# Performance work log

Measured on AMD Instinct MI355X. Metric: run time of the kernel, lower is better.

Reference implementation:

```python
import jax, jax.numpy as jnp
import numpy as np

B, N, D, H = 2, 2048, 1024, 16
DH = D // H
SCALE = DH ** -0.5

def setup_inputs() -> dict:
    key = jax.random.key(0)
    k1, k2, k3 = jax.random.split(key, 3)
    x = jax.random.normal(k1, (B, N, D), dtype=jnp.float32)
    W_qkv = jax.random.normal(k2, (3 * D, D), dtype=jnp.float32) * (D ** -0.5)
    W_out = jax.random.normal(k3, (D, D), dtype=jnp.float32) * (D ** -0.5)
    mask = jnp.tril(jnp.ones((N, N), dtype=jnp.int32))  # causal mask; 0 -> -inf
    return {"x": x, "mask": mask, "W_qkv": W_qkv, "W_out": W_out}

def reference(x, mask, W_qkv, W_out):
    b, n, d = x.shape
    qkv = x @ W_qkv.T                                   # [B,N,3D]
    qkv = qkv.reshape(b, n, 3, H, DH).transpose(2, 0, 3, 1, 4)  # [3,B,H,N,DH]
    q, k, v = qkv[0], qkv[1], qkv[2]
    attn = jnp.einsum('bhqd,bhkd->bhqk', q, k) * SCALE  # [B,H,N,N]
    attn = jnp.where(mask == 0, -jnp.inf, attn)
    attn = jax.nn.softmax(attn, axis=-1)
    out = jnp.einsum('bhqk,bhkd->bhqd', attn, v)        # [B,H,N,DH]
    out = out.transpose(0, 2, 1, 3).reshape(b, n, d)    # [B,N,D]
    return out @ W_out.T
```

## Files before the change

kernel.cpp:

```cpp
#include <hip/hip_runtime.h>
#include <hip/hip_bf16.h>


typedef __hip_bfloat16 bf16;
typedef short bf16x8 __attribute__((ext_vector_type(8)));
typedef short bf16x4 __attribute__((ext_vector_type(4)));
typedef float f32x4 __attribute__((ext_vector_type(4)));

#define QSCALE 0.1803368801111204f

typedef __attribute__((address_space(3))) unsigned int lds_u32;
typedef const __attribute__((address_space(1))) unsigned int glob_u32;

__device__ __forceinline__ void glds16(const void* g, void* l) {
    __builtin_amdgcn_global_load_lds((glob_u32*)g, (lds_u32*)l, 16, 0, 0);
}

__device__ __forceinline__ short f2bf(float f) {
    __hip_bfloat16 h = __float2bfloat16(f);
    return *reinterpret_cast<short*>(&h);
}

__device__ __forceinline__ unsigned pack_bf16(float a, float b) {
    unsigned au = __builtin_bit_cast(unsigned, a) + 0x8000u;
    unsigned bu = __builtin_bit_cast(unsigned, b) + 0x8000u;
    return __builtin_amdgcn_perm(bu, au, 0x07060302u);
}

__global__ void cast_all(const float* __restrict__ x, const float* __restrict__ wqkv,
                         const float* __restrict__ wout,
                         bf16* __restrict__ xb, bf16* __restrict__ wqkvb,
                         bf16* __restrict__ woutb) {
    int i = blockIdx.x * blockDim.x + threadIdx.x;
    const float4* s; short4* d; int o;
    if (i < 1048576)               { s = (const float4*)x;    d = (short4*)xb;    o = i; }
    else if (i < 1835008)          { s = (const float4*)wqkv; d = (short4*)wqkvb; o = i - 1048576; }
    else                           { s = (const float4*)wout; d = (short4*)woutb; o = i - 1835008; }
    float4 f = s[o];
    short4 v;
    v.x = f2bf(f.x); v.y = f2bf(f.y); v.z = f2bf(f.z); v.w = f2bf(f.w);
    d[o] = v;
}

template<int EPI>
__global__ __launch_bounds__(256)
void gemm128(const bf16* __restrict__ A, const bf16* __restrict__ Bt,
             float* __restrict__ Cf,
             bf16* __restrict__ qp, bf16* __restrict__ kp, bf16* __restrict__ vp,
             int K, int Ncols) {
    __shared__ alignas(16) short As[2][4096];
    __shared__ alignas(16) short Bs[2][4096];

    const int tid = threadIdx.x;
    const int wave = tid >> 6, lane = tid & 63;
    const int quad = lane >> 4, l16 = lane & 15;
    const int wm = wave >> 1, wn = wave & 1;
    const int m0 = blockIdx.x * 128;
    const int n0 = blockIdx.y * 128;

    f32x4 acc[4][4] = {};

    const int srow = tid >> 2;
    const int skk  = (((tid & 3) ^ ((tid >> 3) & 3))) * 8;
    const bf16* Ag = A  + (size_t)(m0 + srow) * K + skk;
    const bf16* Bg = Bt + (size_t)(n0 + srow) * K + skk;
    const size_t rowskip = (size_t)64 * K;
    short* Asl = &As[0][0] + tid * 8;
    short* Bsl = &Bs[0][0] + tid * 8;

    const int xk = (quad ^ ((l16 >> 1) & 3)) * 8;
    const int arow = wm * 64 + l16;
    const int brow = wn * 64 + l16;

    const int KI = K >> 5;
    glds16(Ag, Asl);
    glds16(Ag + rowskip, Asl + 2048);
    glds16(Bg, Bsl);
    glds16(Bg + rowskip, Bsl + 2048);
    __syncthreads();

    int buf = 0;
    for (int ki = 0; ki < KI; ++ki) {
        if (ki + 1 < KI) {
            const bf16* ag = Ag + (ki + 1) * 32;
            const bf16* bg = Bg + (ki + 1) * 32;
            short* ad = Asl + (buf ^ 1) * 4096;
            short* bd = Bsl + (buf ^ 1) * 4096;
            glds16(ag, ad);
            glds16(ag + rowskip, ad + 2048);
            glds16(bg, bd);
            glds16(bg + rowskip, bd + 2048);
        }
        const short* ab = &As[buf][0];
        const short* bb = &Bs[buf][0];
        bf16x8 af[4], bf[4];
        #pragma unroll
        for (int mt = 0; mt < 4; ++mt)
            af[mt] = *reinterpret_cast<const bf16x8*>(ab + (arow + mt * 16) * 32 + xk);
        #pragma unroll
        for (int nt = 0; nt < 4; ++nt)
            bf[nt] = *reinterpret_cast<const bf16x8*>(bb + (brow + nt * 16) * 32 + xk);
        #pragma unroll
        for (int mt = 0; mt < 4; ++mt)
            #pragma unroll
            for (int nt = 0; nt < 4; ++nt)
                acc[mt][nt] = __builtin_amdgcn_mfma_f32_16x16x32_bf16(
                    af[mt], bf[nt], acc[mt][nt], 0, 0, 0);
        __syncthreads();
        buf ^= 1;
    }

    #pragma unroll
    for (int mt = 0; mt < 4; ++mt) {
        #pragma unroll
        for (int nt = 0; nt < 4; ++nt) {
            #pragma unroll
            for (int r = 0; r < 4; ++r) {
                int gm = m0 + wm * 64 + mt * 16 + quad * 4 + r;
                int gn = n0 + wn * 64 + nt * 16 + l16;
                float val = acc[mt][nt][r];
                if (EPI == 0) {
                    int sel = gn >> 10, rem = gn & 1023;
                    int h = rem >> 6, dh = rem & 63;
                    int b = gm >> 11, nq = gm & 2047;
                    if (sel == 0) val *= QSCALE;
                    bf16* dst = (sel == 0) ? qp : ((sel == 1) ? kp : vp);
                    dst[((((size_t)b * 16 + h) * 2048) + nq) * 64 + dh] = __float2bfloat16(val);
                } else {
                    Cf[(size_t)gm * Ncols + gn] = val;
                }
            }
        }
    }
}

__global__ __launch_bounds__(256)
void flash_attn(const bf16* __restrict__ Q, const bf16* __restrict__ K,
                const bf16* __restrict__ V, bf16* __restrict__ O) {
    __shared__ alignas(16) short Ks[2][64][72];
    __shared__ alignas(16) short Vt[2][64][68];

    const int tid = threadIdx.x;
    const int wave = tid >> 6, lane = tid & 63;
    const int quad = lane >> 4, l16 = lane & 15;
    const int bh = blockIdx.x;
    const int yy = blockIdx.y;
    const int qt = (yy < 8) ? yy : (15 - (yy & 7));
    const int Q0 = qt * 128;
    const float NEG_INF = -__builtin_inff();

    const bf16* Qb = Q + (size_t)bh * 2048 * 64;
    const bf16* Kb = K + (size_t)bh * 2048 * 64;
    const bf16* Vb = V + (size_t)bh * 2048 * 64;

    const int qrowA = Q0 + wave * 16 + l16;
    const int qrowB = qrowA + 64;
    const bf16x8 qfA0 = *reinterpret_cast<const bf16x8*>(Qb + (size_t)qrowA * 64 + quad * 8);
    const bf16x8 qfA1 = *reinterpret_cast<const bf16x8*>(Qb + (size_t)qrowA * 64 + 32 + quad * 8);
    const bf16x8 qfB0 = *reinterpret_cast<const bf16x8*>(Qb + (size_t)qrowB * 64 + quad * 8);
    const bf16x8 qfB1 = *reinterpret_cast<const bf16x8*>(Qb + (size_t)qrowB * 64 + 32 + quad * 8);

    float lA = 0.f, lB = 0.f;
    f32x4 oA[4] = {}, oB[4] = {};

    const int krow = tid >> 2;
    const int kcol = (tid & 3) * 16;
    const int kb = (tid & 15) * 4;
    const int db = (tid >> 4) * 4;

    {
        bf16x8 a0 = *reinterpret_cast<const bf16x8*>(Kb + (size_t)krow * 64 + kcol);
        bf16x8 a1 = *reinterpret_cast<const bf16x8*>(Kb + (size_t)krow * 64 + kcol + 8);
        bf16x4 L0 = *reinterpret_cast<const bf16x4*>(Vb + (size_t)(kb + 0) * 64 + db);
        bf16x4 L1 = *reinterpret_cast<const bf16x4*>(Vb + (size_t)(kb + 1) * 64 + db);
        bf16x4 L2 = *reinterpret_cast<const bf16x4*>(Vb + (size_t)(kb + 2) * 64 + db);
        bf16x4 L3 = *reinterpret_cast<const bf16x4*>(Vb + (size_t)(kb + 3) * 64 + db);
        *reinterpret_cast<bf16x8*>(&Ks[0][krow][kcol]) = a0;
        *reinterpret_cast<bf16x8*>(&Ks[0][krow][kcol + 8]) = a1;
        #pragma unroll
        for (int j = 0; j < 4; ++j) {
            bf16x4 w; w[0] = L0[j]; w[1] = L1[j]; w[2] = L2[j]; w[3] = L3[j];
            *reinterpret_cast<bf16x4*>(&Vt[0][db + j][kb]) = w;
        }
    }
    __syncthreads();

    int buf = 0;
    for (int j0 = 0; j0 < Q0; j0 += 64) {
        const bf16* Kn = Kb + (size_t)(j0 + 64) * 64;
        const bf16* Vn = Vb + (size_t)(j0 + 64) * 64;
        bf16x8 nk0 = *reinterpret_cast<const bf16x8*>(Kn + (size_t)krow * 64 + kcol);
        bf16x8 nk1 = *reinterpret_cast<const bf16x8*>(Kn + (size_t)krow * 64 + kcol + 8);
        bf16x4 N0 = *reinterpret_cast<const bf16x4*>(Vn + (size_t)(kb + 0) * 64 + db);
        bf16x4 N1 = *reinterpret_cast<const bf16x4*>(Vn + (size_t)(kb + 1) * 64 + db);
        bf16x4 N2 = *reinterpret_cast<const bf16x4*>(Vn + (size_t)(kb + 2) * 64 + db);
        bf16x4 N3 = *reinterpret_cast<const bf16x4*>(Vn + (size_t)(kb + 3) * 64 + db);

        bf16x4 pkA[4], pkB[4];
        #pragma unroll
        for (int t = 0; t < 4; ++t) {
            bf16x8 k0 = *reinterpret_cast<const bf16x8*>(&Ks[buf][16 * t + l16][quad * 8]);
            bf16x8 k1 = *reinterpret_cast<const bf16x8*>(&Ks[buf][16 * t + l16][32 + quad * 8]);
            f32x4 sA = {}, sB = {};
            sA = __builtin_amdgcn_mfma_f32_16x16x32_bf16(k0, qfA0, sA, 0, 0, 0);
            sA = __builtin_amdgcn_mfma_f32_16x16x32_bf16(k1, qfA1, sA, 0, 0, 0);
            sB = __builtin_amdgcn_mfma_f32_16x16x32_bf16(k0, qfB0, sB, 0, 0, 0);
            sB = __builtin_amdgcn_mfma_f32_16x16x32_bf16(k1, qfB1, sB, 0, 0, 0);
            float a0 = __builtin_amdgcn_exp2f(sA[0]);
            float a1 = __builtin_amdgcn_exp2f(sA[1]);
            float a2 = __builtin_amdgcn_exp2f(sA[2]);
            float a3 = __builtin_amdgcn_exp2f(sA[3]);
            float b0 = __builtin_amdgcn_exp2f(sB[0]);
            float b1 = __builtin_amdgcn_exp2f(sB[1]);
            float b2 = __builtin_amdgcn_exp2f(sB[2]);
            float b3 = __builtin_amdgcn_exp2f(sB[3]);
            lA += (a0 + a1) + (a2 + a3);
            lB += (b0 + b1) + (b2 + b3);
            unsigned* pa = reinterpret_cast<unsigned*>(&pkA[t]);
            pa[0] = pack_bf16(a0, a1); pa[1] = pack_bf16(a2, a3);
            unsigned* pb = reinterpret_cast<unsigned*>(&pkB[t]);
            pb[0] = pack_bf16(b0, b1); pb[1] = pack_bf16(b2, b3);
        }

        #pragma unroll
        for (int t = 0; t < 4; ++t) {
            #pragma unroll
            for (int dt = 0; dt < 4; ++dt) {
                bf16x4 vf = *reinterpret_cast<const bf16x4*>(
                    &Vt[buf][dt * 16 + l16][t * 16 + quad * 4]);
                oA[dt] = __builtin_amdgcn_mfma_f32_16x16x16bf16_1k(vf, pkA[t], oA[dt], 0, 0, 0);
                oB[dt] = __builtin_amdgcn_mfma_f32_16x16x16bf16_1k(vf, pkB[t], oB[dt], 0, 0, 0);
            }
        }

        *reinterpret_cast<bf16x8*>(&Ks[buf ^ 1][krow][kcol]) = nk0;
        *reinterpret_cast<bf16x8*>(&Ks[buf ^ 1][krow][kcol + 8]) = nk1;
        #pragma unroll
        for (int j = 0; j < 4; ++j) {
            bf16x4 w; w[0] = N0[j]; w[1] = N1[j]; w[2] = N2[j]; w[3] = N3[j];
            *reinterpret_cast<bf16x4*>(&Vt[buf ^ 1][db + j][kb]) = w;
        }
        __syncthreads();
        buf ^= 1;
    }

    {
        const bf16* Kn = Kb + (size_t)(Q0 + 64) * 64;
        const bf16* Vn = Vb + (size_t)(Q0 + 64) * 64;
        bf16x8 nk0 = *reinterpret_cast<const bf16x8*>(Kn + (size_t)krow * 64 + kcol);
        bf16x8 nk1 = *reinterpret_cast<const bf16x8*>(Kn + (size_t)krow * 64 + kcol + 8);
        bf16x4 N0 = *reinterpret_cast<const bf16x4*>(Vn + (size_t)(kb + 0) * 64 + db);
        bf16x4 N1 = *reinterpret_cast<const bf16x4*>(Vn + (size_t)(kb + 1) * 64 + db);
        bf16x4 N2 = *reinterpret_cast<const bf16x4*>(Vn + (size_t)(kb + 2) * 64 + db);
        bf16x4 N3 = *reinterpret_cast<const bf16x4*>(Vn + (size_t)(kb + 3) * 64 + db);

        bf16x4 pkA[4], pkB[4];
        #pragma unroll
        for (int t = 0; t < 4; ++t) {
            bf16x8 k0 = *reinterpret_cast<const bf16x8*>(&Ks[buf][16 * t + l16][quad * 8]);
            bf16x8 k1 = *reinterpret_cast<const bf16x8*>(&Ks[buf][16 * t + l16][32 + quad * 8]);
            f32x4 sB = {};
            sB = __builtin_amdgcn_mfma_f32_16x16x32_bf16(k0, qfB0, sB, 0, 0, 0);
            sB = __builtin_amdgcn_mfma_f32_16x16x32_bf16(k1, qfB1, sB, 0, 0, 0);
            float b0 = __builtin_amdgcn_exp2f(sB[0]);
            float b1 = __builtin_amdgcn_exp2f(sB[1]);
            float b2 = __builtin_amdgcn_exp2f(sB[2]);
            float b3 = __builtin_amdgcn_exp2f(sB[3]);
            lB += (b0 + b1) + (b2 + b3);
            unsigned* pb = reinterpret_cast<unsigned*>(&pkB[t]);
            pb[0] = pack_bf16(b0, b1); pb[1] = pack_bf16(b2, b3);
            if (t <= wave) {
                f32x4 sA = {};
                sA = __builtin_amdgcn_mfma_f32_16x16x32_bf16(k0, qfA0, sA, 0, 0, 0);
                sA = __builtin_amdgcn_mfma_f32_16x16x32_bf16(k1, qfA1, sA, 0, 0, 0);
                if (t == wave) {
                    #pragma unroll
                    for (int r = 0; r < 4; ++r)
                        if (quad * 4 + r > l16) sA[r] = NEG_INF;
                }
                float a0 = __builtin_amdgcn_exp2f(sA[0]);
                float a1 = __builtin_amdgcn_exp2f(sA[1]);
                float a2 = __builtin_amdgcn_exp2f(sA[2]);
                float a3 = __builtin_amdgcn_exp2f(sA[3]);
                lA += (a0 + a1) + (a2 + a3);
                unsigned* pa = reinterpret_cast<unsigned*>(&pkA[t]);
                pa[0] = pack_bf16(a0, a1); pa[1] = pack_bf16(a2, a3);
            }
        }
        #pragma unroll
        for (int t = 0; t < 4; ++t) {
            #pragma unroll
            for (int dt = 0; dt < 4; ++dt) {
                bf16x4 vf = *reinterpret_cast<const bf16x4*>(
                    &Vt[buf][dt * 16 + l16][t * 16 + quad * 4]);
                oB[dt] = __builtin_amdgcn_mfma_f32_16x16x16bf16_1k(vf, pkB[t], oB[dt], 0, 0, 0);
                if (t <= wave)
                    oA[dt] = __builtin_amdgcn_mfma_f32_16x16x16bf16_1k(vf, pkA[t], oA[dt], 0, 0, 0);
            }
        }

        *reinterpret_cast<bf16x8*>(&Ks[buf ^ 1][krow][kcol]) = nk0;
        *reinterpret_cast<bf16x8*>(&Ks[buf ^ 1][krow][kcol + 8]) = nk1;
        #pragma unroll
        for (int j = 0; j < 4; ++j) {
            bf16x4 w; w[0] = N0[j]; w[1] = N1[j]; w[2] = N2[j]; w[3] = N3[j];
            *reinterpret_cast<bf16x4*>(&Vt[buf ^ 1][db + j][kb]) = w;
        }
        __syncthreads();
        buf ^= 1;
    }

    {
        bf16x4 pkB[4];
        #pragma unroll
        for (int t = 0; t < 4; ++t) {
            if (t <= wave) {
                bf16x8 k0 = *reinterpret_cast<const bf16x8*>(&Ks[buf][16 * t + l16][quad * 8]);
                bf16x8 k1 = *reinterpret_cast<const bf16x8*>(&Ks[buf][16 * t + l16][32 + quad * 8]);
                f32x4 sB = {};
                sB = __builtin_amdgcn_mfma_f32_16x16x32_bf16(k0, qfB0, sB, 0, 0, 0);
                sB = __builtin_amdgcn_mfma_f32_16x16x32_bf16(k1, qfB1, sB, 0, 0, 0);
                if (t == wave) {
                    #pragma unroll
                    for (int r = 0; r < 4; ++r)
                        if (quad * 4 + r > l16) sB[r] = NEG_INF;
                }
                float b0 = __builtin_amdgcn_exp2f(sB[0]);
                float b1 = __builtin_amdgcn_exp2f(sB[1]);
                float b2 = __builtin_amdgcn_exp2f(sB[2]);
                float b3 = __builtin_amdgcn_exp2f(sB[3]);
                lB += (b0 + b1) + (b2 + b3);
                unsigned* pb = reinterpret_cast<unsigned*>(&pkB[t]);
                pb[0] = pack_bf16(b0, b1); pb[1] = pack_bf16(b2, b3);
            }
        }
        #pragma unroll
        for (int t = 0; t < 4; ++t) {
            if (t <= wave) {
                #pragma unroll
                for (int dt = 0; dt < 4; ++dt) {
                    bf16x4 vf = *reinterpret_cast<const bf16x4*>(
                        &Vt[buf][dt * 16 + l16][t * 16 + quad * 4]);
                    oB[dt] = __builtin_amdgcn_mfma_f32_16x16x16bf16_1k(vf, pkB[t], oB[dt], 0, 0, 0);
                }
            }
        }
    }

    lA += __shfl_xor(lA, 16, 64);
    lA += __shfl_xor(lA, 32, 64);
    lB += __shfl_xor(lB, 16, 64);
    lB += __shfl_xor(lB, 32, 64);
    const float invA = 1.f / lA;
    const float invB = 1.f / lB;

    const int b = bh >> 4, h = bh & 15;
    bf16* orowA = O + ((size_t)b * 2048 + qrowA) * 1024 + h * 64;
    bf16* orowB = O + ((size_t)b * 2048 + qrowB) * 1024 + h * 64;
    #pragma unroll
    for (int dt = 0; dt < 4; ++dt) {
        bf16x4 wA, wB;
        unsigned* ua = reinterpret_cast<unsigned*>(&wA);
        ua[0] = pack_bf16(oA[dt][0] * invA, oA[dt][1] * invA);
        ua[1] = pack_bf16(oA[dt][2] * invA, oA[dt][3] * invA);
        *reinterpret_cast<bf16x4*>(orowA + dt * 16 + quad * 4) = wA;
        unsigned* ub = reinterpret_cast<unsigned*>(&wB);
        ub[0] = pack_bf16(oB[dt][0] * invB, oB[dt][1] * invB);
        ub[1] = pack_bf16(oB[dt][2] * invB, oB[dt][3] * invB);
        *reinterpret_cast<bf16x4*>(orowB + dt * 16 + quad * 4) = wB;
    }
}

extern "C" void kernel_launch(void* const* d_in, const int* in_sizes, int n_in,
                              void* d_out, int out_size, void* d_ws, size_t ws_size,
                              hipStream_t stream) {
    const float* x    = (const float*)d_in[0];
    const float* Wqkv = (const float*)d_in[2];
    const float* Wout = (const float*)d_in[3];
    float* out = (float*)d_out;

    char* ws = (char*)d_ws;
    bf16* x_bf    = (bf16*)(ws);
    bf16* wqkv_bf = (bf16*)(ws + 8388608);
    bf16* wout_bf = (bf16*)(ws + 14680064);
    bf16* q       = (bf16*)(ws + 16777216);
    bf16* k       = (bf16*)(ws + 25165824);
    bf16* v       = (bf16*)(ws + 33554432);
    bf16* ao      = (bf16*)(ws + 41943040);

    cast_all<<<8192, 256, 0, stream>>>(x, Wqkv, Wout, x_bf, wqkv_bf, wout_bf);
    gemm128<0><<<dim3(32, 24), 256, 0, stream>>>(x_bf, wqkv_bf, nullptr, q, k, v, 1024, 3072);
    flash_attn<<<dim3(32, 16), 256, 0, stream>>>(q, k, v, ao);
    gemm128<1><<<dim3(32, 8), 256, 0, stream>>>(ao, wout_bf, out, nullptr, nullptr, nullptr, 1024, 1024);
}
```

Before: 181.3 us.

## Split flash attention query tile across 8 waves, separate K/V loader threads

The attention block grows from 256 to 512 threads, so each wave now owns 16 query rows instead of 32 (two row groups A and B). Half the threads load and transpose V while the other half load K, instead of every thread doing both. This halves per-wave register state and serial MFMA work, which should raise latency hiding through more waves per block. The cost is more waves contending for barriers and less reuse of each K/V LDS fragment per wave.

```diff
diff --git a/kernel.cpp b/kernel.cpp
--- a/kernel.cpp
+++ b/kernel.cpp
@@ -134,7 +134,7 @@
     }
 }
 
-__global__ __launch_bounds__(256)
+__global__ __launch_bounds__(512)
 void flash_attn(const bf16* __restrict__ Q, const bf16* __restrict__ K,
                 const bf16* __restrict__ V, bf16* __restrict__ O) {
     __shared__ alignas(16) short Ks[2][64][72];
@@ -153,34 +153,35 @@
     const bf16* Kb = K + (size_t)bh * 2048 * 64;
     const bf16* Vb = V + (size_t)bh * 2048 * 64;
 
-    const int qrowA = Q0 + wave * 16 + l16;
-    const int qrowB = qrowA + 64;
-    const bf16x8 qfA0 = *reinterpret_cast<const bf16x8*>(Qb + (size_t)qrowA * 64 + quad * 8);
-    const bf16x8 qfA1 = *reinterpret_cast<const bf16x8*>(Qb + (size_t)qrowA * 64 + 32 + quad * 8);
-    const bf16x8 qfB0 = *reinterpret_cast<const bf16x8*>(Qb + (size_t)qrowB * 64 + quad * 8);
-    const bf16x8 qfB1 = *reinterpret_cast<const bf16x8*>(Qb + (size_t)qrowB * 64 + 32 + quad * 8);
-
-    float lA = 0.f, lB = 0.f;
-    f32x4 oA[4] = {}, oB[4] = {};
-
-    const int krow = tid >> 2;
-    const int kcol = (tid & 3) * 16;
-    const int kb = (tid & 15) * 4;
-    const int db = (tid >> 4) * 4;
+    const int qrow = Q0 + wave * 16 + l16;
+    const bf16x8 qf0 = *reinterpret_cast<const bf16x8*>(Qb + (size_t)qrow * 64 + quad * 8);
+    const bf16x8 qf1 = *reinterpret_cast<const bf16x8*>(Qb + (size_t)qrow * 64 + 32 + quad * 8);
+
+    float l = 0.f;
+    f32x4 o[4] = {};
+
+    const int t2   = tid & 255;
+    const int krow = t2 >> 2;
+    const int kcol = (t2 & 3) * 16;
+    const int kb   = (t2 & 15) * 4;
+    const int db   = (t2 >> 4) * 4;
 
     {
-        bf16x8 a0 = *reinterpret_cast<const bf16x8*>(Kb + (size_t)krow * 64 + kcol);
-        bf16x8 a1 = *reinterpret_cast<const bf16x8*>(Kb + (size_t)krow * 64 + kcol + 8);
-        bf16x4 L0 = *reinterpret_cast<const bf16x4*>(Vb + (size_t)(kb + 0) * 64 + db);
-        bf16x4 L1 = *reinterpret_cast<const bf16x4*>(Vb + (size_t)(kb + 1) * 64 + db);
-        bf16x4 L2 = *reinterpret_cast<const bf16x4*>(Vb + (size_t)(kb + 2) * 64 + db);
-        bf16x4 L3 = *reinterpret_cast<const bf16x4*>(Vb + (size_t)(kb + 3) * 64 + db);
-        *reinterpret_cast<bf16x8*>(&Ks[0][krow][kcol]) = a0;
-        *reinterpret_cast<bf16x8*>(&Ks[0][krow][kcol + 8]) = a1;
-        #pragma unroll
-        for (int j = 0; j < 4; ++j) {
-            bf16x4 w; w[0] = L0[j]; w[1] = L1[j]; w[2] = L2[j]; w[3] = L3[j];
-            *reinterpret_cast<bf16x4*>(&Vt[0][db + j][kb]) = w;
+        if (tid < 256) {
+            bf16x4 L0 = *reinterpret_cast<const bf16x4*>(Vb + (size_t)(kb + 0) * 64 + db);
+            bf16x4 L1 = *reinterpret_cast<const bf16x4*>(Vb + (size_t)(kb + 1) * 64 + db);
+            bf16x4 L2 = *reinterpret_cast<const bf16x4*>(Vb + (size_t)(kb + 2) * 64 + db);
+            bf16x4 L3 = *reinterpret_cast<const bf16x4*>(Vb + (size_t)(kb + 3) * 64 + db);
+            #pragma unroll
+            for (int j = 0; j < 4; ++j) {
+                bf16x4 w; w[0] = L0[j]; w[1] = L1[j]; w[2] = L2[j]; w[3] = L3[j];
+                *reinterpret_cast<bf16x4*>(&Vt[0][db + j][kb]) = w;
+            }
+        } else {
+            bf16x8 a0 = *reinterpret_cast<const bf16x8*>(Kb + (size_t)krow * 64 + kcol);
+            bf16x8 a1 = *reinterpret_cast<const bf16x8*>(Kb + (size_t)krow * 64 + kcol + 8);
+            *reinterpret_cast<bf16x8*>(&Ks[0][krow][kcol]) = a0;
+            *reinterpret_cast<bf16x8*>(&Ks[0][krow][kcol + 8]) = a1;
         }
     }
     __syncthreads();
@@ -189,37 +190,33 @@
     for (int j0 = 0; j0 < Q0; j0 += 64) {
         const bf16* Kn = Kb + (size_t)(j0 + 64) * 64;
         const bf16* Vn = Vb + (size_t)(j0 + 64) * 64;
-        bf16x8 nk0 = *reinterpret_cast<const bf16x8*>(Kn + (size_t)krow * 64 + kcol);
-        bf16x8 nk1 = *reinterpret_cast<const bf16x8*>(Kn + (size_t)krow * 64 + kcol + 8);
-        bf16x4 N0 = *reinterpret_cast<const bf16x4*>(Vn + (size_t)(kb + 0) * 64 + db);
-        bf16x4 N1 = *reinterpret_cast<const bf16x4*>(Vn + (size_t)(kb + 1) * 64 + db);
-        bf16x4 N2 = *reinterpret_cast<const bf16x4*>(Vn + (size_t)(kb + 2) * 64 + db);
-        bf16x4 N3 = *reinterpret_cast<const bf16x4*>(Vn + (size_t)(kb + 3) * 64 + db);
-
-        bf16x4 pkA[4], pkB[4];
+        bf16x8 nk0, nk1;
+        bf16x4 N0, N1, N2, N3;
+        if (tid < 256) {
+            N0 = *reinterpret_cast<const bf16x4*>(Vn + (size_t)(kb + 0) * 64 + db);
+            N1 = *reinterpret_cast<const bf16x4*>(Vn + (size_t)(kb + 1) * 64 + db);
+            N2 = *reinterpret_cast<const bf16x4*>(Vn + (size_t)(kb + 2) * 64 + db);
+            N3 = *reinterpret_cast<const bf16x4*>(Vn + (size_t)(kb + 3) * 64 + db);
+        } else {
+            nk0 = *reinterpret_cast<const bf16x8*>(Kn + (size_t)krow * 64 + kcol);
+            nk1 = *reinterpret_cast<const bf16x8*>(Kn + (size_t)krow * 64 + kcol + 8);
+        }
+
+        bf16x4 pk[4];
         #pragma unroll
         for (int t = 0; t < 4; ++t) {
             bf16x8 k0 = *reinterpret_cast<const bf16x8*>(&Ks[buf][16 * t + l16][quad * 8]);
             bf16x8 k1 = *reinterpret_cast<const bf16x8*>(&Ks[buf][16 * t + l16][32 + quad * 8]);
-            f32x4 sA = {}, sB = {};
-            sA = __builtin_amdgcn_mfma_f32_16x16x32_bf16(k0, qfA0, sA, 0, 0, 0);
-            sA = __builtin_amdgcn_mfma_f32_16x16x32_bf16(k1, qfA1, sA, 0, 0, 0);
-            sB = __builtin_amdgcn_mfma_f32_16x16x32_bf16(k0, qfB0, sB, 0, 0, 0);
-            sB = __builtin_amdgcn_mfma_f32_16x16x32_bf16(k1, qfB1, sB, 0, 0, 0);
-            float a0 = __builtin_amdgcn_exp2f(sA[0]);
-            float a1 = __builtin_amdgcn_exp2f(sA[1]);
-            float a2 = __builtin_amdgcn_exp2f(sA[2]);
-            float a3 = __builtin_amdgcn_exp2f(sA[3]);
-            float b0 = __builtin_amdgcn_exp2f(sB[0]);
-            float b1 = __builtin_amdgcn_exp2f(sB[1]);
-            float b2 = __builtin_amdgcn_exp2f(sB[2]);
-            float b3 = __builtin_amdgcn_exp2f(sB[3]);
-            lA += (a0 + a1) + (a2 + a3);
-            lB += (b0 + b1) + (b2 + b3);
-            unsigned* pa = reinterpret_cast<unsigned*>(&pkA[t]);
-            pa[0] = pack_bf16(a0, a1); pa[1] = pack_bf16(a2, a3);
-            unsigned* pb = reinterpret_cast<unsigned*>(&pkB[t]);
-            pb[0] = pack_bf16(b0, b1); pb[1] = pack_bf16(b2, b3);
+            f32x4 s = {};
+            s = __builtin_amdgcn_mfma_f32_16x16x32_bf16(k0, qf0, s, 0, 0, 0);
+            s = __builtin_amdgcn_mfma_f32_16x16x32_bf16(k1, qf1, s, 0, 0, 0);
+            float e0 = __builtin_amdgcn_exp2f(s[0]);
+            float e1 = __builtin_amdgcn_exp2f(s[1]);
+            float e2 = __builtin_amdgcn_exp2f(s[2]);
+            float e3 = __builtin_amdgcn_exp2f(s[3]);
+            l += (e0 + e1) + (e2 + e3);
+            unsigned* p = reinterpret_cast<unsigned*>(&pk[t]);
+            p[0] = pack_bf16(e0, e1); p[1] = pack_bf16(e2, e3);
         }
 
         #pragma unroll
@@ -228,17 +225,19 @@
             for (int dt = 0; dt < 4; ++dt) {
                 bf16x4 vf = *reinterpret_cast<const bf16x4*>(
                     &Vt[buf][dt * 16 + l16][t * 16 + quad * 4]);
-                oA[dt] = __builtin_amdgcn_mfma_f32_16x16x16bf16_1k(vf, pkA[t], oA[dt], 0, 0, 0);
-                oB[dt] = __builtin_amdgcn_mfma_f32_16x16x16bf16_1k(vf, pkB[t], oB[dt], 0, 0, 0);
-            }
-        }
-
-        *reinterpret_cast<bf16x8*>(&Ks[buf ^ 1][krow][kcol]) = nk0;
-        *reinterpret_cast<bf16x8*>(&Ks[buf ^ 1][krow][kcol + 8]) = nk1;
-        #pragma unroll
-        for (int j = 0; j < 4; ++j) {
-            bf16x4 w; w[0] = N0[j]; w[1] = N1[j]; w[2] = N2[j]; w[3] = N3[j];
-            *reinterpret_cast<bf16x4*>(&Vt[buf ^ 1][db + j][kb]) = w;
+                o[dt] = __builtin_amdgcn_mfma_f32_16x16x16bf16_1k(vf, pk[t], o[dt], 0, 0, 0);
+            }
+        }
+
+        if (tid < 256) {
+            #pragma unroll
+            for (int j = 0; j < 4; ++j) {
+                bf16x4 w; w[0] = N0[j]; w[1] = N1[j]; w[2] = N2[j]; w[3] = N3[j];
+                *reinterpret_cast<bf16x4*>(&Vt[buf ^ 1][db + j][kb]) = w;
+            }
+        } else {
+            *reinterpret_cast<bf16x8*>(&Ks[buf ^ 1][krow][kcol]) = nk0;
+            *reinterpret_cast<bf16x8*>(&Ks[buf ^ 1][krow][kcol + 8]) = nk1;
         }
         __syncthreads();
         buf ^= 1;
@@ -247,127 +246,119 @@
     {
         const bf16* Kn = Kb + (size_t)(Q0 + 64) * 64;
         const bf16* Vn = Vb + (size_t)(Q0 + 64) * 64;
-        bf16x8 nk0 = *reinterpret_cast<const bf16x8*>(Kn + (size_t)krow * 64 + kcol);
-        bf16x8 nk1 = *reinterpret_cast<const bf16x8*>(Kn + (size_t)krow * 64 + kcol + 8);
-        bf16x4 N0 = *reinterpret_cast<const bf16x4*>(Vn + (size_t)(kb + 0) * 64 + db);
-        bf16x4 N1 = *reinterpret_cast<const bf16x4*>(Vn + (size_t)(kb + 1) * 64 + db);
-        bf16x4 N2 = *reinterpret_cast<const bf16x4*>(Vn + (size_t)(kb + 2) * 64 + db);
-        bf16x4 N3 = *reinterpret_cast<const bf16x4*>(Vn + (size_t)(kb + 3) * 64 + db);
-
-        bf16x4 pkA[4], pkB[4];
-        #pragma unroll
-        for (int t = 0; t < 4; ++t) {
-            bf16x8 k0 = *reinterpret_cast<const bf16x8*>(&Ks[buf][16 * t + l16][quad * 8]);
-            bf16x8 k1 = *reinterpret_cast<const bf16x8*>(&Ks[buf][16 * t + l16][32 + quad * 8]);
-            f32x4 sB = {};
-            sB = __builtin_amdgcn_mfma_f32_16x16x32_bf16(k0, qfB0, sB, 0, 0, 0);
-            sB = __builtin_amdgcn_mfma_f32_16x16x32_bf16(k1, qfB1, sB, 0, 0, 0);
-            float b0 = __builtin_amdgcn_exp2f(sB[0]);
-            float b1 = __builtin_amdgcn_exp2f(sB[1]);
-            float b2 = __builtin_amdgcn_exp2f(sB[2]);
-            float b3 = __builtin_amdgcn_exp2f(sB[3]);
-            lB += (b0 + b1) + (b2 + b3);
-            unsigned* pb = reinterpret_cast<unsigned*>(&pkB[t]);
-            pb[0] = pack_bf16(b0, b1); pb[1] = pack_bf16(b2, b3);
-            if (t <= wave) {
-                f32x4 sA = {};
-                sA = __builtin_amdgcn_mfma_f32_16x16x32_bf16(k0, qfA0, sA, 0, 0, 0);
-                sA = __builtin_amdgcn_mfma_f32_16x16x32_bf16(k1, qfA1, sA, 0, 0, 0);
-                if (t == wave) {
+        bf16x8 nk0, nk1;
+        bf16x4 N0, N1, N2, N3;
+        if (tid < 256) {
+            N0 = *reinterpret_cast<const bf16x4*>(Vn + (size_t)(kb + 0) * 64 + db);
+            N1 = *reinterpret_cast<const bf16x4*>(Vn + (size_t)(kb + 1) * 64 + db);
+            N2 = *reinterpret_cast<const bf16x4*>(Vn + (size_t)(kb + 2) * 64 + db);
+            N3 = *reinterpret_cast<const bf16x4*>(Vn + (size_t)(kb + 3) * 64 + db);
+        } else {
+            nk0 = *reinterpret_cast<const bf16x8*>(Kn + (size_t)krow * 64 + kcol);
+            nk1 = *reinterpret_cast<const bf16x8*>(Kn + (size_t)krow * 64 + kcol + 8);
+        }
+
+        const bool full = (wave >= 4);
+        bf16x4 pk[4];
+        #pragma unroll
+        for (int t = 0; t < 4; ++t) {
+            if (full || t <= wave) {
+                bf16x8 k0 = *reinterpret_cast<const bf16x8*>(&Ks[buf][16 * t + l16][quad * 8]);
+                bf16x8 k1 = *reinterpret_cast<const bf16x8*>(&Ks[buf][16 * t + l16][32 + quad * 8]);
+                f32x4 s = {};
+                s = __builtin_amdgcn_mfma_f32_16x16x32_bf16(k0, qf0, s, 0, 0, 0);
+                s = __builtin_amdgcn_mfma_f32_16x16x32_bf16(k1, qf1, s, 0, 0, 0);
+                if (!full && t == wave) {
                     #pragma unroll
                     for (int r = 0; r < 4; ++r)
-                        if (quad * 4 + r > l16) sA[r] = NEG_INF;
-                }
-                float a0 = __builtin_amdgcn_exp2f(sA[0]);
-                float a1 = __builtin_amdgcn_exp2f(sA[1]);
-                float a2 = __builtin_amdgcn_exp2f(sA[2]);
-                float a3 = __builtin_amdgcn_exp2f(sA[3]);
-                lA += (a0 + a1) + (a2 + a3);
-                unsigned* pa = reinterpret_cast<unsigned*>(&pkA[t]);
-                pa[0] = pack_bf16(a0, a1); pa[1] = pack_bf16(a2, a3);
-            }
-        }
-        #pragma unroll
-        for (int t = 0; t < 4; ++t) {
-            #pragma unroll
-            for (int dt = 0; dt < 4; ++dt) {
-                bf16x4 vf = *reinterpret_cast<const bf16x4*>(
-                    &Vt[buf][dt * 16 + l16][t * 16 + quad * 4]);
-                oB[dt] = __builtin_amdgcn_mfma_f32_16x16x16bf16_1k(vf, pkB[t], oB[dt], 0, 0, 0);
-                if (t <= wave)
-                    oA[dt] = __builtin_amdgcn_mfma_f32_16x16x16bf16_1k(vf, pkA[t], oA[dt], 0, 0, 0);
-            }
-        }
-
-        *reinterpret_cast<bf16x8*>(&Ks[buf ^ 1][krow][kcol]) = nk0;
-        *reinterpret_cast<bf16x8*>(&Ks[buf ^ 1][krow][kcol + 8]) = nk1;
-        #pragma unroll
-        for (int j = 0; j < 4; ++j) {
-            bf16x4 w; w[0] = N0[j]; w[1] = N1[j]; w[2] = N2[j]; w[3] = N3[j];
-            *reinterpret_cast<bf16x4*>(&Vt[buf ^ 1][db + j][kb]) = w;
-        }
-        __syncthreads();
-        buf ^= 1;
-    }
-
-    {
-        bf16x4 pkB[4];
-        #pragma unroll
-        for (int t = 0; t < 4; ++t) {
-            if (t <= wave) {
-                bf16x8 k0 = *reinterpret_cast<const bf16x8*>(&Ks[buf][16 * t + l16][quad * 8]);
-                bf16x8 k1 = *reinterpret_cast<const bf16x8*>(&Ks[buf][16 * t + l16][32 + quad * 8]);
-                f32x4 sB = {};
-                sB = __builtin_amdgcn_mfma_f32_16x16x32_bf16(k0, qfB0, sB, 0, 0, 0);
-                sB = __builtin_amdgcn_mfma_f32_16x16x32_bf16(k1, qfB1, sB, 0, 0, 0);
-                if (t == wave) {
-                    #pragma unroll
-                    for (int r = 0; r < 4; ++r)
-                        if (quad * 4 + r > l16) sB[r] = NEG_INF;
-                }
-                float b0 = __builtin_amdgcn_exp2f(sB[0]);
-                float b1 = __builtin_amdgcn_exp2f(sB[1]);
-                float b2 = __builtin_amdgcn_exp2f(sB[2]);
-                float b3 = __builtin_amdgcn_exp2f(sB[3]);
-                lB += (b0 + b1) + (b2 + b3);
-                unsigned* pb = reinterpret_cast<unsigned*>(&pkB[t]);
-                pb[0] = pack_bf16(b0, b1); pb[1] = pack_bf16(b2, b3);
-            }
-        }
-        #pragma unroll
-        for (int t = 0; t < 4; ++t) {
-            if (t <= wave) {
+                        if (quad * 4 + r > l16) s[r] = NEG_INF;
+                }
+                float e0 = __builtin_amdgcn_exp2f(s[0]);
+                float e1 = __builtin_amdgcn_exp2f(s[1]);
+                float e2 = __builtin_amdgcn_exp2f(s[2]);
+                float e3 = __builtin_amdgcn_exp2f(s[3]);
+                l += (e0 + e1) + (e2 + e3);
+                unsigned* p = reinterpret_cast<unsigned*>(&pk[t]);
+                p[0] = pack_bf16(e0, e1); p[1] = pack_bf16(e2, e3);
+            }
+        }
+        #pragma unroll
+        for (int t = 0; t < 4; ++t) {
+            if (full || t <= wave) {
                 #pragma unroll
                 for (int dt = 0; dt < 4; ++dt) {
                     bf16x4 vf = *reinterpret_cast<const bf16x4*>(
                         &Vt[buf][dt * 16 + l16][t * 16 + quad * 4]);
-                    oB[dt] = __builtin_amdgcn_mfma_f32_16x16x16bf16_1k(vf, pkB[t], oB[dt], 0, 0, 0);
-                }
-            }
-        }
-    }
-
-    lA += __shfl_xor(lA, 16, 64);
-    lA += __shfl_xor(lA, 32, 64);
-    lB += __shfl_xor(lB, 16, 64);
-    lB += __shfl_xor(lB, 32, 64);
-    const float invA = 1.f / lA;
-    const float invB = 1.f / lB;
+                    o[dt] = __builtin_amdgcn_mfma_f32_16x16x16bf16_1k(vf, pk[t], o[dt], 0, 0, 0);
+                }
+            }
+        }
+
+        if (tid < 256) {
+            #pragma unroll
+            for (int j = 0; j < 4; ++j) {
+                bf16x4 w; w[0] = N0[j]; w[1] = N1[j]; w[2] = N2[j]; w[3] = N3[j];
+                *reinterpret_cast<bf16x4*>(&Vt[buf ^ 1][db + j][kb]) = w;
+            }
+        } else {
+            *reinterpret_cast<bf16x8*>(&Ks[buf ^ 1][krow][kcol]) = nk0;
+            *reinterpret_cast<bf16x8*>(&Ks[buf ^ 1][krow][kcol + 8]) = nk1;
+        }
+        __syncthreads();
+        buf ^= 1;
+    }
+
+    if (wave >= 4) {
+        const int w4 = wave - 4;
+        bf16x4 pk[4];
+        #pragma unroll
+        for (int t = 0; t < 4; ++t) {
+            if (t <= w4) {
+                bf16x8 k0 = *reinterpret_cast<const bf16x8*>(&Ks[buf][16 * t + l16][quad * 8]);
+                bf16x8 k1 = *reinterpret_cast<const bf16x8*>(&Ks[buf][16 * t + l16][32 + quad * 8]);
+                f32x4 s = {};
+                s = __builtin_amdgcn_mfma_f32_16x16x32_bf16(k0, qf0, s, 0, 0, 0);
+                s = __builtin_amdgcn_mfma_f32_16x16x32_bf16(k1, qf1, s, 0, 0, 0);
+                if (t == w4) {
+                    #pragma unroll
+                    for (int r = 0; r < 4; ++r)
+                        if (quad * 4 + r > l16) s[r] = NEG_INF;
+                }
+                float e0 = __builtin_amdgcn_exp2f(s[0]);
+                float e1 = __builtin_amdgcn_exp2f(s[1]);
+                float e2 = __builtin_amdgcn_exp2f(s[2]);
+                float e3 = __builtin_amdgcn_exp2f(s[3]);
+                l += (e0 + e1) + (e2 + e3);
+                unsigned* p = reinterpret_cast<unsigned*>(&pk[t]);
+                p[0] = pack_bf16(e0, e1); p[1] = pack_bf16(e2, e3);
+            }
+        }
+        #pragma unroll
+        for (int t = 0; t < 4; ++t) {
+            if (t <= w4) {
+                #pragma unroll
+                for (int dt = 0; dt < 4; ++dt) {
+                    bf16x4 vf = *reinterpret_cast<const bf16x4*>(
+                        &Vt[buf][dt * 16 + l16][t * 16 + quad * 4]);
+                    o[dt] = __builtin_amdgcn_mfma_f32_16x16x16bf16_1k(vf, pk[t], o[dt], 0, 0, 0);
+                }
+            }
+        }
+    }
+
+    l += __shfl_xor(l, 16, 64);
+    l += __shfl_xor(l, 32, 64);
+    const float inv = 1.f / l;
 
     const int b = bh >> 4, h = bh & 15;
-    bf16* orowA = O + ((size_t)b * 2048 + qrowA) * 1024 + h * 64;
-    bf16* orowB = O + ((size_t)b * 2048 + qrowB) * 1024 + h * 64;
+    bf16* orow = O + ((size_t)b * 2048 + qrow) * 1024 + h * 64;
     #pragma unroll
     for (int dt = 0; dt < 4; ++dt) {
-        bf16x4 wA, wB;
-        unsigned* ua = reinterpret_cast<unsigned*>(&wA);
-        ua[0] = pack_bf16(oA[dt][0] * invA, oA[dt][1] * invA);
-        ua[1] = pack_bf16(oA[dt][2] * invA, oA[dt][3] * invA);
-        *reinterpret_cast<bf16x4*>(orowA + dt * 16 + quad * 4) = wA;
-        unsigned* ub = reinterpret_cast<unsigned*>(&wB);
-        ub[0] = pack_bf16(oB[dt][0] * invB, oB[dt][1] * invB);
-        ub[1] = pack_bf16(oB[dt][2] * invB, oB[dt][3] * invB);
-        *reinterpret_cast<bf16x4*>(orowB + dt * 16 + quad * 4) = wB;
+        bf16x4 w;
+        unsigned* u = reinterpret_cast<unsigned*>(&w);
+        u[0] = pack_bf16(o[dt][0] * inv, o[dt][1] * inv);
+        u[1] = pack_bf16(o[dt][2] * inv, o[dt][3] * inv);
+        *reinterpret_cast<bf16x4*>(orow + dt * 16 + quad * 4) = w;
     }
 }
 
@@ -390,6 +381,6 @@
 
     cast_all<<<8192, 256, 0, stream>>>(x, Wqkv, Wout, x_bf, wqkv_bf, wout_bf);
     gemm128<0><<<dim3(32, 24), 256, 0, stream>>>(x_bf, wqkv_bf, nullptr, q, k, v, 1024, 3072);
-    flash_attn<<<dim3(32, 16), 256, 0, stream>>>(q, k, v, ao);
+    flash_attn<<<dim3(32, 16), 512, 0, stream>>>(q, k, v, ao);
     gemm128<1><<<dim3(32, 8), 256, 0, stream>>>(ao, wout_bf, out, nullptr, nullptr, nullptr, 1024, 1024);
 }
```

Measured after the change: 184.3 us. Within noise of the previous version (+1.6%).

## Widen flash attention KV tiles to 128 rows and merge diagonal blocks

Applied to the files above, without the earlier changes.

Doubles the K/V tile staged in shared memory per iteration from 64 to 128 keys. This halves the number of barrier and prefetch rounds and merges the two causal diagonal tail blocks into a single masked 128-key block. It also adds a launch-bounds occupancy hint of 2 blocks. In exchange it roughly doubles LDS use and the registers held for prefetched tiles, which may reduce occupancy or cause spills.

```diff
diff --git a/kernel.cpp b/kernel.cpp
--- a/kernel.cpp
+++ b/kernel.cpp
@@ -134,11 +134,11 @@
     }
 }
 
-__global__ __launch_bounds__(256)
+__global__ __launch_bounds__(256, 2)
 void flash_attn(const bf16* __restrict__ Q, const bf16* __restrict__ K,
                 const bf16* __restrict__ V, bf16* __restrict__ O) {
-    __shared__ alignas(16) short Ks[2][64][72];
-    __shared__ alignas(16) short Vt[2][64][68];
+    __shared__ alignas(16) short Ks[2][128][72];
+    __shared__ alignas(16) short Vt[2][64][132];
 
     const int tid = threadIdx.x;
     const int wave = tid >> 6, lane = tid & 63;
@@ -165,40 +165,52 @@
 
     const int krow = tid >> 2;
     const int kcol = (tid & 3) * 16;
-    const int kb = (tid & 15) * 4;
-    const int db = (tid >> 4) * 4;
+    const int kb   = (tid & 15) * 4;
+    const int db   = (tid >> 4) * 4;
 
     {
-        bf16x8 a0 = *reinterpret_cast<const bf16x8*>(Kb + (size_t)krow * 64 + kcol);
-        bf16x8 a1 = *reinterpret_cast<const bf16x8*>(Kb + (size_t)krow * 64 + kcol + 8);
-        bf16x4 L0 = *reinterpret_cast<const bf16x4*>(Vb + (size_t)(kb + 0) * 64 + db);
-        bf16x4 L1 = *reinterpret_cast<const bf16x4*>(Vb + (size_t)(kb + 1) * 64 + db);
-        bf16x4 L2 = *reinterpret_cast<const bf16x4*>(Vb + (size_t)(kb + 2) * 64 + db);
-        bf16x4 L3 = *reinterpret_cast<const bf16x4*>(Vb + (size_t)(kb + 3) * 64 + db);
-        *reinterpret_cast<bf16x8*>(&Ks[0][krow][kcol]) = a0;
-        *reinterpret_cast<bf16x8*>(&Ks[0][krow][kcol + 8]) = a1;
-        #pragma unroll
-        for (int j = 0; j < 4; ++j) {
-            bf16x4 w; w[0] = L0[j]; w[1] = L1[j]; w[2] = L2[j]; w[3] = L3[j];
-            *reinterpret_cast<bf16x4*>(&Vt[0][db + j][kb]) = w;
+        #pragma unroll
+        for (int g = 0; g < 2; ++g) {
+            const bf16* kr = Kb + (size_t)(g * 64 + krow) * 64 + kcol;
+            *reinterpret_cast<bf16x8*>(&Ks[0][g * 64 + krow][kcol])     = *reinterpret_cast<const bf16x8*>(kr);
+            *reinterpret_cast<bf16x8*>(&Ks[0][g * 64 + krow][kcol + 8]) = *reinterpret_cast<const bf16x8*>(kr + 8);
+        }
+        #pragma unroll
+        for (int g = 0; g < 2; ++g) {
+            const int kbg = g * 64 + kb;
+            bf16x4 L0 = *reinterpret_cast<const bf16x4*>(Vb + (size_t)(kbg + 0) * 64 + db);
+            bf16x4 L1 = *reinterpret_cast<const bf16x4*>(Vb + (size_t)(kbg + 1) * 64 + db);
+            bf16x4 L2 = *reinterpret_cast<const bf16x4*>(Vb + (size_t)(kbg + 2) * 64 + db);
+            bf16x4 L3 = *reinterpret_cast<const bf16x4*>(Vb + (size_t)(kbg + 3) * 64 + db);
+            #pragma unroll
+            for (int j = 0; j < 4; ++j) {
+                bf16x4 w; w[0] = L0[j]; w[1] = L1[j]; w[2] = L2[j]; w[3] = L3[j];
+                *reinterpret_cast<bf16x4*>(&Vt[0][db + j][kbg]) = w;
+            }
         }
     }
     __syncthreads();
 
     int buf = 0;
-    for (int j0 = 0; j0 < Q0; j0 += 64) {
-        const bf16* Kn = Kb + (size_t)(j0 + 64) * 64;
-        const bf16* Vn = Vb + (size_t)(j0 + 64) * 64;
-        bf16x8 nk0 = *reinterpret_cast<const bf16x8*>(Kn + (size_t)krow * 64 + kcol);
-        bf16x8 nk1 = *reinterpret_cast<const bf16x8*>(Kn + (size_t)krow * 64 + kcol + 8);
-        bf16x4 N0 = *reinterpret_cast<const bf16x4*>(Vn + (size_t)(kb + 0) * 64 + db);
-        bf16x4 N1 = *reinterpret_cast<const bf16x4*>(Vn + (size_t)(kb + 1) * 64 + db);
-        bf16x4 N2 = *reinterpret_cast<const bf16x4*>(Vn + (size_t)(kb + 2) * 64 + db);
-        bf16x4 N3 = *reinterpret_cast<const bf16x4*>(Vn + (size_t)(kb + 3) * 64 + db);
-
-        bf16x4 pkA[4], pkB[4];
-        #pragma unroll
-        for (int t = 0; t < 4; ++t) {
+    for (int j0 = 0; j0 < Q0; j0 += 128) {
+        const bf16* Kn = Kb + (size_t)(j0 + 128) * 64;
+        const bf16* Vn = Vb + (size_t)(j0 + 128) * 64;
+        bf16x8 nk[2][2];
+        bf16x4 NV[2][4];
+        #pragma unroll
+        for (int g = 0; g < 2; ++g) {
+            const bf16* kr = Kn + (size_t)(g * 64 + krow) * 64 + kcol;
+            nk[g][0] = *reinterpret_cast<const bf16x8*>(kr);
+            nk[g][1] = *reinterpret_cast<const bf16x8*>(kr + 8);
+            const int kbg = g * 64 + kb;
+            #pragma unroll
+            for (int j = 0; j < 4; ++j)
+                NV[g][j] = *reinterpret_cast<const bf16x4*>(Vn + (size_t)(kbg + j) * 64 + db);
+        }
+
+        bf16x4 pkA[8], pkB[8];
+        #pragma unroll
+        for (int t = 0; t < 8; ++t) {
             bf16x8 k0 = *reinterpret_cast<const bf16x8*>(&Ks[buf][16 * t + l16][quad * 8]);
             bf16x8 k1 = *reinterpret_cast<const bf16x8*>(&Ks[buf][16 * t + l16][32 + quad * 8]);
             f32x4 sA = {}, sB = {};
@@ -223,7 +235,7 @@
         }
 
         #pragma unroll
-        for (int t = 0; t < 4; ++t) {
+        for (int t = 0; t < 8; ++t) {
             #pragma unroll
             for (int dt = 0; dt < 4; ++dt) {
                 bf16x4 vf = *reinterpret_cast<const bf16x4*>(
@@ -233,94 +245,34 @@
             }
         }
 
-        *reinterpret_cast<bf16x8*>(&Ks[buf ^ 1][krow][kcol]) = nk0;
-        *reinterpret_cast<bf16x8*>(&Ks[buf ^ 1][krow][kcol + 8]) = nk1;
-        #pragma unroll
-        for (int j = 0; j < 4; ++j) {
-            bf16x4 w; w[0] = N0[j]; w[1] = N1[j]; w[2] = N2[j]; w[3] = N3[j];
-            *reinterpret_cast<bf16x4*>(&Vt[buf ^ 1][db + j][kb]) = w;
+        #pragma unroll
+        for (int g = 0; g < 2; ++g) {
+            *reinterpret_cast<bf16x8*>(&Ks[buf ^ 1][g * 64 + krow][kcol])     = nk[g][0];
+            *reinterpret_cast<bf16x8*>(&Ks[buf ^ 1][g * 64 + krow][kcol + 8]) = nk[g][1];
+            const int kbg = g * 64 + kb;
+            #pragma unroll
+            for (int j = 0; j < 4; ++j) {
+                bf16x4 w; w[0] = NV[g][0][j]; w[1] = NV[g][1][j]; w[2] = NV[g][2][j]; w[3] = NV[g][3][j];
+                *reinterpret_cast<bf16x4*>(&Vt[buf ^ 1][db + j][kbg]) = w;
+            }
         }
         __syncthreads();
         buf ^= 1;
     }
 
     {
-        const bf16* Kn = Kb + (size_t)(Q0 + 64) * 64;
-        const bf16* Vn = Vb + (size_t)(Q0 + 64) * 64;
-        bf16x8 nk0 = *reinterpret_cast<const bf16x8*>(Kn + (size_t)krow * 64 + kcol);
-        bf16x8 nk1 = *reinterpret_cast<const bf16x8*>(Kn + (size_t)krow * 64 + kcol + 8);
-        bf16x4 N0 = *reinterpret_cast<const bf16x4*>(Vn + (size_t)(kb + 0) * 64 + db);
-        bf16x4 N1 = *reinterpret_cast<const bf16x4*>(Vn + (size_t)(kb + 1) * 64 + db);
-        bf16x4 N2 = *reinterpret_cast<const bf16x4*>(Vn + (size_t)(kb + 2) * 64 + db);
-        bf16x4 N3 = *reinterpret_cast<const bf16x4*>(Vn + (size_t)(kb + 3) * 64 + db);
-
-        bf16x4 pkA[4], pkB[4];
-        #pragma unroll
-        for (int t = 0; t < 4; ++t) {
-            bf16x8 k0 = *reinterpret_cast<const bf16x8*>(&Ks[buf][16 * t + l16][quad * 8]);
-            bf16x8 k1 = *reinterpret_cast<const bf16x8*>(&Ks[buf][16 * t + l16][32 + quad * 8]);
-            f32x4 sB = {};
-            sB = __builtin_amdgcn_mfma_f32_16x16x32_bf16(k0, qfB0, sB, 0, 0, 0);
-            sB = __builtin_amdgcn_mfma_f32_16x16x32_bf16(k1, qfB1, sB, 0, 0, 0);
-            float b0 = __builtin_amdgcn_exp2f(sB[0]);
-            float b1 = __builtin_amdgcn_exp2f(sB[1]);
-            float b2 = __builtin_amdgcn_exp2f(sB[2]);
-            float b3 = __builtin_amdgcn_exp2f(sB[3]);
-            lB += (b0 + b1) + (b2 + b3);
-            unsigned* pb = reinterpret_cast<unsigned*>(&pkB[t]);
-            pb[0] = pack_bf16(b0, b1); pb[1] = pack_bf16(b2, b3);
-            if (t <= wave) {
-                f32x4 sA = {};
-                sA = __builtin_amdgcn_mfma_f32_16x16x32_bf16(k0, qfA0, sA, 0, 0, 0);
-                sA = __builtin_amdgcn_mfma_f32_16x16x32_bf16(k1, qfA1, sA, 0, 0, 0);
-                if (t == wave) {
-                    #pragma unroll
-                    for (int r = 0; r < 4; ++r)
-                        if (quad * 4 + r > l16) sA[r] = NEG_INF;
-                }
-                float a0 = __builtin_amdgcn_exp2f(sA[0]);
-                float a1 = __builtin_amdgcn_exp2f(sA[1]);
-                float a2 = __builtin_amdgcn_exp2f(sA[2]);
-                float a3 = __builtin_amdgcn_exp2f(sA[3]);
-                lA += (a0 + a1) + (a2 + a3);
-                unsigned* pa = reinterpret_cast<unsigned*>(&pkA[t]);
-                pa[0] = pack_bf16(a0, a1); pa[1] = pack_bf16(a2, a3);
-            }
-        }
-        #pragma unroll
-        for (int t = 0; t < 4; ++t) {
-            #pragma unroll
-            for (int dt = 0; dt < 4; ++dt) {
-                bf16x4 vf = *reinterpret_cast<const bf16x4*>(
-                    &Vt[buf][dt * 16 + l16][t * 16 + quad * 4]);
-                oB[dt] = __builtin_amdgcn_mfma_f32_16x16x16bf16_1k(vf, pkB[t], oB[dt], 0, 0, 0);
-                if (t <= wave)
-                    oA[dt] = __builtin_amdgcn_mfma_f32_16x16x16bf16_1k(vf, pkA[t], oA[dt], 0, 0, 0);
-            }
-        }
-
-        *reinterpret_cast<bf16x8*>(&Ks[buf ^ 1][krow][kcol]) = nk0;
-        *reinterpret_cast<bf16x8*>(&Ks[buf ^ 1][krow][kcol + 8]) = nk1;
-        #pragma unroll
-        for (int j = 0; j < 4; ++j) {
-            bf16x4 w; w[0] = N0[j]; w[1] = N1[j]; w[2] = N2[j]; w[3] = N3[j];
-            *reinterpret_cast<bf16x4*>(&Vt[buf ^ 1][db + j][kb]) = w;
-        }
-        __syncthreads();
-        buf ^= 1;
-    }
-
-    {
-        bf16x4 pkB[4];
-        #pragma unroll
-        for (int t = 0; t < 4; ++t) {
-            if (t <= wave) {
+        bf16x4 pkA[8], pkB[8];
+        #pragma unroll
+        for (int t = 0; t < 8; ++t) {
+            const bool actB = (t <= wave + 4);
+            const bool actA = (t <= wave);
+            if (actB) {
                 bf16x8 k0 = *reinterpret_cast<const bf16x8*>(&Ks[buf][16 * t + l16][quad * 8]);
                 bf16x8 k1 = *reinterpret_cast<const bf16x8*>(&Ks[buf][16 * t + l16][32 + quad * 8]);
                 f32x4 sB = {};
                 sB = __builtin_amdgcn_mfma_f32_16x16x32_bf16(k0, qfB0, sB, 0, 0, 0);
                 sB = __builtin_amdgcn_mfma_f32_16x16x32_bf16(k1, qfB1, sB, 0, 0, 0);
-                if (t == wave) {
+                if (t == wave + 4) {
                     #pragma unroll
                     for (int r = 0; r < 4; ++r)
                         if (quad * 4 + r > l16) sB[r] = NEG_INF;
@@ -332,16 +284,35 @@
                 lB += (b0 + b1) + (b2 + b3);
                 unsigned* pb = reinterpret_cast<unsigned*>(&pkB[t]);
                 pb[0] = pack_bf16(b0, b1); pb[1] = pack_bf16(b2, b3);
-            }
-        }
-        #pragma unroll
-        for (int t = 0; t < 4; ++t) {
-            if (t <= wave) {
+                if (actA) {
+                    f32x4 sA = {};
+                    sA = __builtin_amdgcn_mfma_f32_16x16x32_bf16(k0, qfA0, sA, 0, 0, 0);
+                    sA = __builtin_amdgcn_mfma_f32_16x16x32_bf16(k1, qfA1, sA, 0, 0, 0);
+                    if (t == wave) {
+                        #pragma unroll
+                        for (int r = 0; r < 4; ++r)
+                            if (quad * 4 + r > l16) sA[r] = NEG_INF;
+                    }
+                    float a0 = __builtin_amdgcn_exp2f(sA[0]);
+                    float a1 = __builtin_amdgcn_exp2f(sA[1]);
+                    float a2 = __builtin_amdgcn_exp2f(sA[2]);
+                    float a3 = __builtin_amdgcn_exp2f(sA[3]);
+                    lA += (a0 + a1) + (a2 + a3);
+                    unsigned* pa = reinterpret_cast<unsigned*>(&pkA[t]);
+                    pa[0] = pack_bf16(a0, a1); pa[1] = pack_bf16(a2, a3);
+                }
+            }
+        }
+        #pragma unroll
+        for (int t = 0; t < 8; ++t) {
+            if (t <= wave + 4) {
                 #pragma unroll
                 for (int dt = 0; dt < 4; ++dt) {
                     bf16x4 vf = *reinterpret_cast<const bf16x4*>(
                         &Vt[buf][dt * 16 + l16][t * 16 + quad * 4]);
                     oB[dt] = __builtin_amdgcn_mfma_f32_16x16x16bf16_1k(vf, pkB[t], oB[dt], 0, 0, 0);
+                    if (t <= wave)
+                        oA[dt] = __builtin_amdgcn_mfma_f32_16x16x16bf16_1k(vf, pkA[t], oA[dt], 0, 0, 0);
                 }
             }
         }
```

Result: no change. 178.9 us (-1.3%).
